# Optimization experiments

Hardware: AMD Instinct MI355X
Metric: run time of the kernel (lower is better)

Reference implementation:

```python
import jax, jax.numpy as jnp
import numpy as np
import math

D_MODEL = 768
N_HEADS = 12
D_HEAD = D_MODEL // N_HEADS


def setup_inputs() -> dict:
    key = jax.random.key(0)
    ks = jax.random.split(key, 5)
    x = jax.random.normal(ks[0], (2, 4096, D_MODEL), dtype=jnp.float32)
    s = 1.0 / math.sqrt(D_MODEL)
    W_qkv = jax.random.normal(ks[1], (D_MODEL, 3 * D_MODEL), dtype=jnp.float32) * s
    b_qkv = jnp.zeros((3 * D_MODEL,), dtype=jnp.float32)
    W_out = jax.random.normal(ks[2], (D_MODEL, D_MODEL), dtype=jnp.float32) * s
    b_out = jnp.zeros((D_MODEL,), dtype=jnp.float32)
    return {"x": x, "W_qkv": W_qkv, "b_qkv": b_qkv, "W_out": W_out, "b_out": b_out}


def reference(x, W_qkv, b_qkv, W_out, b_out):
    B, T, C = x.shape
    H, Dh = N_HEADS, D_HEAD
    qkv = x @ W_qkv + b_qkv                      # [B,T,3C]
    q, k, v = jnp.split(qkv, 3, axis=-1)
    q = q.reshape(B, T, H, Dh).transpose(0, 2, 1, 3)  # [B,H,T,Dh]
    k = k.reshape(B, T, H, Dh).transpose(0, 2, 1, 3)
    v = v.reshape(B, T, H, Dh).transpose(0, 2, 1, 3)
    att = jnp.einsum('bhqd,bhkd->bhqk', q, k) * (1.0 / math.sqrt(Dh))
    causal = jnp.tril(jnp.ones((T, T), dtype=bool))
    att = jnp.where(causal, att, -jnp.inf)
    att = jax.nn.softmax(att, axis=-1)
    out = jnp.einsum('bhqk,bhkd->bhqd', att, v)  # [B,H,T,Dh]
    out = out.transpose(0, 2, 1, 3).reshape(B, T, C)
    return out @ W_out + b_out
```

## Files before the change

kernel.cpp:

```cpp
#include <hip/hip_runtime.h>
#include <hip/hip_bf16.h>
#include <cstdint>

#define NH 12
#define DH 64
#define TSEQ 4096
#define BATCH 2
#define CDIM 768
#define MROWS (BATCH*TSEQ)

typedef __bf16 bf16x8 __attribute__((ext_vector_type(8)));
typedef __bf16 bf16x4 __attribute__((ext_vector_type(4)));
typedef bf16x8 bf16x8_a __attribute__((may_alias));
typedef bf16x4 bf16x4_a __attribute__((may_alias));
typedef float f32x4 __attribute__((ext_vector_type(4)));

__device__ __forceinline__ uint16_t f2bu(float f) {
  uint32_t u = __float_as_uint(f);
  u += 0x7fffu + ((u >> 16) & 1u);
  return (uint16_t)(u >> 16);
}

__device__ __forceinline__ float bu2f(uint16_t x) {
  return __uint_as_float(((uint32_t)x) << 16);
}

__device__ __forceinline__ void gload_lds16(const void* g, void* l) {
  __builtin_amdgcn_global_load_lds(
      (const __attribute__((address_space(1))) void*)g,
      (__attribute__((address_space(3))) void*)l, 16, 0, 0);
}

__global__ void cast_f32_bf16(const float* __restrict__ in, uint16_t* __restrict__ out, int n4) {
  int i = blockIdx.x * blockDim.x + threadIdx.x;
  int stride = gridDim.x * blockDim.x;
  for (; i < n4; i += stride) {
    float4 v = ((const float4*)in)[i];
    ushort4 o;
    o.x = f2bu(v.x); o.y = f2bu(v.y); o.z = f2bu(v.z); o.w = f2bu(v.w);
    ((ushort4*)out)[i] = o;
  }
}

__global__ void transpose_cast(const float* __restrict__ w, uint16_t* __restrict__ wt, int K, int N) {
  __shared__ float tile[32][33];
  int kb = blockIdx.x * 32, nb = blockIdx.y * 32;
  int tx = threadIdx.x & 31, ty = threadIdx.x >> 5;
  #pragma unroll
  for (int r = ty; r < 32; r += 8) tile[r][tx] = w[(size_t)(kb + r) * N + nb + tx];
  __syncthreads();
  #pragma unroll
  for (int r = ty; r < 32; r += 8) wt[(size_t)(nb + r) * K + kb + tx] = f2bu(tile[tx][r]);
}

__global__ __launch_bounds__(256) void gemm_qkv(
    const uint16_t* __restrict__ A, const uint16_t* __restrict__ Bt,
    const float* __restrict__ bias,
    uint16_t* __restrict__ q, uint16_t* __restrict__ k, uint16_t* __restrict__ v,
    int N, int K) {
  __shared__ uint16_t As[128 * 32];
  __shared__ uint16_t Bs[128 * 32];
  int tid = threadIdx.x;
  int w = tid >> 6, l = tid & 63;
  int lg = l >> 4, lr = l & 15;
  int mb = blockIdx.x * 128, nb = blockIdx.y * 128;
  int wr = (w >> 1) * 64, wc = (w & 1) * 64;
  f32x4 acc[4][4] = {};
  int srow = tid >> 2, scol = (tid & 3) * 8;
  const uint16_t* Ag = A + (size_t)(mb + srow) * K + scol;
  const uint16_t* Bg = Bt + (size_t)(nb + srow) * K + scol;
  char* AsB = (char*)As + (size_t)w * 1024;
  char* BsB = (char*)Bs + (size_t)w * 1024;
  size_t rowskip = (size_t)64 * K;
  for (int kb = 0; kb < K; kb += 32) {
    __syncthreads();
    gload_lds16(Ag + kb, AsB);
    gload_lds16(Ag + kb + rowskip, AsB + 4096);
    gload_lds16(Bg + kb, BsB);
    gload_lds16(Bg + kb + rowskip, BsB + 4096);
    __syncthreads();
    bf16x8 af[4], bfr[4];
    #pragma unroll
    for (int i = 0; i < 4; ++i)
      af[i] = *(const bf16x8_a*)(const void*)(As + (wr + i * 16 + lr) * 32 + lg * 8);
    #pragma unroll
    for (int i = 0; i < 4; ++i)
      bfr[i] = *(const bf16x8_a*)(const void*)(Bs + (wc + i * 16 + lr) * 32 + lg * 8);
    #pragma unroll
    for (int mi = 0; mi < 4; ++mi)
      #pragma unroll
      for (int ni = 0; ni < 4; ++ni)
        acc[mi][ni] = __builtin_amdgcn_mfma_f32_16x16x32_bf16(af[mi], bfr[ni], acc[mi][ni], 0, 0, 0);
  }
  #pragma unroll
  for (int mi = 0; mi < 4; ++mi) {
    #pragma unroll
    for (int ni = 0; ni < 4; ++ni) {
      int gm0 = mb + wr + mi * 16 + lg * 4;
      int gn = nb + wc + ni * 16 + lr;
      int which = gn / CDIM;
      int cc = gn - which * CDIM;
      int hh = cc >> 6, d = cc & 63;
      float bs = bias[gn];
      if (which == 2) {
        int b0 = gm0 >> 12, t0 = gm0 & 4095;
        ushort4 pk;
        pk.x = f2bu(acc[mi][ni][0] + bs);
        pk.y = f2bu(acc[mi][ni][1] + bs);
        pk.z = f2bu(acc[mi][ni][2] + bs);
        pk.w = f2bu(acc[mi][ni][3] + bs);
        *(ushort4*)&v[(((size_t)(b0 * NH + hh)) * DH + d) * TSEQ + t0] = pk;
      } else {
        uint16_t* dst = which ? k : q;
        float sc = which ? 1.0f : 0.1803368801111204f;
        #pragma unroll
        for (int j = 0; j < 4; ++j) {
          int gm = gm0 + j;
          int bb = gm >> 12, t = gm & 4095;
          float val = (acc[mi][ni][j] + bs) * sc;
          dst[(((size_t)(bb * NH + hh)) * TSEQ + t) * DH + d] = f2bu(val);
        }
      }
    }
  }
}

__global__ __launch_bounds__(256) void gemm_out(
    const uint16_t* __restrict__ A, const uint16_t* __restrict__ Bt,
    const float* __restrict__ bias, float* __restrict__ outf, int N, int K) {
  __shared__ uint16_t As[128 * 32];
  __shared__ uint16_t Bs[64 * 32];
  int tid = threadIdx.x;
  int w = tid >> 6, l = tid & 63;
  int lg = l >> 4, lr = l & 15;
  int mb = blockIdx.x * 128, nb = blockIdx.y * 64;
  int wr = w * 32;
  f32x4 acc[2][4] = {};
  int srow = tid >> 2, scol = (tid & 3) * 8;
  const uint16_t* Ag = A + (size_t)(mb + srow) * K + scol;
  const uint16_t* Bg = Bt + (size_t)(nb + srow) * K + scol;
  char* AsB = (char*)As + (size_t)w * 1024;
  char* BsB = (char*)Bs + (size_t)w * 1024;
  size_t rowskip = (size_t)64 * K;
  for (int kb = 0; kb < K; kb += 32) {
    __syncthreads();
    gload_lds16(Ag + kb, AsB);
    gload_lds16(Ag + kb + rowskip, AsB + 4096);
    gload_lds16(Bg + kb, BsB);
    __syncthreads();
    bf16x8 af[2], bfr[4];
    #pragma unroll
    for (int i = 0; i < 2; ++i)
      af[i] = *(const bf16x8_a*)(const void*)(As + (wr + i * 16 + lr) * 32 + lg * 8);
    #pragma unroll
    for (int i = 0; i < 4; ++i)
      bfr[i] = *(const bf16x8_a*)(const void*)(Bs + (i * 16 + lr) * 32 + lg * 8);
    #pragma unroll
    for (int mi = 0; mi < 2; ++mi)
      #pragma unroll
      for (int ni = 0; ni < 4; ++ni)
        acc[mi][ni] = __builtin_amdgcn_mfma_f32_16x16x32_bf16(af[mi], bfr[ni], acc[mi][ni], 0, 0, 0);
  }
  #pragma unroll
  for (int mi = 0; mi < 2; ++mi) {
    #pragma unroll
    for (int ni = 0; ni < 4; ++ni) {
      #pragma unroll
      for (int j = 0; j < 4; ++j) {
        int gm = mb + wr + mi * 16 + lg * 4 + j;
        int gn = nb + ni * 16 + lr;
        outf[(size_t)gm * N + gn] = acc[mi][ni][j] + bias[gn];
      }
    }
  }
}

__global__ __launch_bounds__(256) void attn_part(
    const uint16_t* __restrict__ Q, const uint16_t* __restrict__ K,
    const uint16_t* __restrict__ Vt, uint16_t* __restrict__ O,
    uint16_t* __restrict__ Pbuf, float* __restrict__ Plsum) {
  int gid = blockIdx.x;
  int widx = gid / 24, bh = gid - widx * 24;
  int qt, t0, t1, chunk;
  bool direct;
  if (widx < 32) {
    qt = 31 - (widx >> 1); chunk = widx & 1; direct = false;
    t0 = chunk ? (qt + 1) : 0;
    t1 = chunk ? (2 * qt + 1) : qt;
  } else {
    qt = 47 - widx; chunk = 0; direct = true;
    t0 = 0; t1 = 2 * qt + 1;
  }
  int b = bh / NH, hd = bh - b * NH;
  size_t base = (size_t)bh * TSEQ * DH;
  int tid = threadIdx.x, w = tid >> 6, lane = tid & 63;
  int lg = lane >> 4, lr = lane & 15;
  __shared__ __align__(16) uint16_t Ks[64 * 64];
  __shared__ __align__(16) uint16_t Vs[64 * 64];
  __shared__ uint16_t Ps[4][16 * 64];
  char* pw = (char*)Ps[w];
  int srow = tid >> 3;
  int schunk = (tid & 7) ^ (srow & 7);
  const uint16_t* Kg0 = K + base + (size_t)srow * DH + schunk * 8;
  const uint16_t* Vg0 = Vt + base + (size_t)srow * TSEQ + schunk * 8;
  char* KsB = (char*)Ks + w * 1024;
  char* VsB = (char*)Vs + w * 1024;
  int swzA = (lg ^ (lr & 7)) << 4;
  int swzB = swzA ^ 64;

  int qb = qt * 128;
  int qgA = qb + w * 16 + lr;
  int qgB = qgA + 64;
  bf16x8 qA0 = *(const bf16x8_a*)(const void*)(Q + base + (size_t)qgA * DH + lg * 8);
  bf16x8 qA1 = *(const bf16x8_a*)(const void*)(Q + base + (size_t)qgA * DH + 32 + lg * 8);
  bf16x8 qB0 = *(const bf16x8_a*)(const void*)(Q + base + (size_t)qgB * DH + lg * 8);
  bf16x8 qB1 = *(const bf16x8_a*)(const void*)(Q + base + (size_t)qgB * DH + 32 + lg * 8);
  f32x4 oA[4] = {}, oB[4] = {};
  float lA = 0.f, lB = 0.f;
  int lg4 = lg * 4;
  int pofs = (lg & 1) * 8;

  for (int t = t0; t <= t1; ++t) {
    __syncthreads();
    {
      const uint16_t* kg_ = Kg0 + (size_t)t * (64 * DH);
      const uint16_t* vg_ = Vg0 + (size_t)t * 64;
      gload_lds16(kg_,           KsB);
      gload_lds16(kg_ + 32 * DH, KsB + 4096);
      gload_lds16(vg_,                     VsB);
      gload_lds16(vg_ + (size_t)32 * TSEQ, VsB + 4096);
    }
    __syncthreads();
    bool doA = (t <= 2 * qt);
    int kb0 = t * 64;
    f32x4 sA[4], sB[4];
    __builtin_amdgcn_s_setprio(1);
    #pragma unroll
    for (int ni = 0; ni < 4; ++ni) {
      const char* kbp = (const char*)Ks + (ni * 16 + lr) * 128;
      bf16x8 kf0 = *(const bf16x8_a*)(kbp + swzA);
      bf16x8 kf1 = *(const bf16x8_a*)(kbp + swzB);
      f32x4 s = {};
      s = __builtin_amdgcn_mfma_f32_16x16x32_bf16(kf0, qB0, s, 0, 0, 0);
      s = __builtin_amdgcn_mfma_f32_16x16x32_bf16(kf1, qB1, s, 0, 0, 0);
      sB[ni] = s;
      if (doA) {
        f32x4 sa = {};
        sa = __builtin_amdgcn_mfma_f32_16x16x32_bf16(kf0, qA0, sa, 0, 0, 0);
        sa = __builtin_amdgcn_mfma_f32_16x16x32_bf16(kf1, qA1, sa, 0, 0, 0);
        sA[ni] = sa;
      }
    }
    __builtin_amdgcn_s_setprio(0);
    bf16x8 pfA0, pfA1;
    if (doA) {
      if (t == 2 * qt) {
        int thr = qgA - kb0 - lg4;
        #pragma unroll
        for (int ni = 0; ni < 4; ++ni)
          #pragma unroll
          for (int j = 0; j < 4; ++j)
            sA[ni][j] = (16 * ni + j <= thr) ? sA[ni][j] : -1e30f;
      }
      #pragma unroll
      for (int ni = 0; ni < 4; ++ni) {
        float p0 = __builtin_amdgcn_exp2f(sA[ni][0]);
        float p1 = __builtin_amdgcn_exp2f(sA[ni][1]);
        float p2 = __builtin_amdgcn_exp2f(sA[ni][2]);
        float p3 = __builtin_amdgcn_exp2f(sA[ni][3]);
        lA += (p0 + p1) + (p2 + p3);
        bf16x4 pk;
        pk[0] = (__bf16)p0; pk[1] = (__bf16)p1; pk[2] = (__bf16)p2; pk[3] = (__bf16)p3;
        int chunkc = (2 * ni + (lg >> 1)) ^ (lr & 7);
        *(bf16x4_a*)(pw + lr * 128 + chunkc * 16 + pofs) = pk;
      }
      pfA0 = *(const bf16x8_a*)(pw + lr * 128 + swzA);
      pfA1 = *(const bf16x8_a*)(pw + lr * 128 + swzB);
    }
    {
      if (t == 2 * qt + 1) {
        int thr = qgB - kb0 - lg4;
        #pragma unroll
        for (int ni = 0; ni < 4; ++ni)
          #pragma unroll
          for (int j = 0; j < 4; ++j)
            sB[ni][j] = (16 * ni + j <= thr) ? sB[ni][j] : -1e30f;
      }
      #pragma unroll
      for (int ni = 0; ni < 4; ++ni) {
        float p0 = __builtin_amdgcn_exp2f(sB[ni][0]);
        float p1 = __builtin_amdgcn_exp2f(sB[ni][1]);
        float p2 = __builtin_amdgcn_exp2f(sB[ni][2]);
        float p3 = __builtin_amdgcn_exp2f(sB[ni][3]);
        lB += (p0 + p1) + (p2 + p3);
        bf16x4 pk;
        pk[0] = (__bf16)p0; pk[1] = (__bf16)p1; pk[2] = (__bf16)p2; pk[3] = (__bf16)p3;
        int chunkc = (2 * ni + (lg >> 1)) ^ (lr & 7);
        *(bf16x4_a*)(pw + lr * 128 + chunkc * 16 + pofs) = pk;
      }
    }
    bf16x8 pfB0 = *(const bf16x8_a*)(pw + lr * 128 + swzA);
    bf16x8 pfB1 = *(const bf16x8_a*)(pw + lr * 128 + swzB);
    __builtin_amdgcn_s_setprio(1);
    #pragma unroll
    for (int nd = 0; nd < 4; ++nd) {
      const char* vb = (const char*)Vs + (nd * 16 + lr) * 128;
      bf16x8 vf0 = *(const bf16x8_a*)(vb + swzA);
      bf16x8 vf1 = *(const bf16x8_a*)(vb + swzB);
      oB[nd] = __builtin_amdgcn_mfma_f32_16x16x32_bf16(pfB0, vf0, oB[nd], 0, 0, 0);
      oB[nd] = __builtin_amdgcn_mfma_f32_16x16x32_bf16(pfB1, vf1, oB[nd], 0, 0, 0);
      if (doA) {
        oA[nd] = __builtin_amdgcn_mfma_f32_16x16x32_bf16(pfA0, vf0, oA[nd], 0, 0, 0);
        oA[nd] = __builtin_amdgcn_mfma_f32_16x16x32_bf16(pfA1, vf1, oA[nd], 0, 0, 0);
      }
    }
    __builtin_amdgcn_s_setprio(0);
  }

  lA += __shfl_xor(lA, 16, 64); lA += __shfl_xor(lA, 32, 64);
  lB += __shfl_xor(lB, 16, 64); lB += __shfl_xor(lB, 32, 64);
  if (direct) {
    float riA = 1.0f / lA, riB = 1.0f / lB;
    #pragma unroll
    for (int j = 0; j < 4; ++j) {
      float rvA = __shfl(riA, (lane & 48) | (lg4 + j), 64);
      float rvB = __shfl(riB, (lane & 48) | (lg4 + j), 64);
      int tA = qb + w * 16 + lg4 + j;
      size_t pA = (size_t)(b * TSEQ + tA) * CDIM + hd * DH + lr;
      size_t pB = pA + (size_t)64 * CDIM;
      #pragma unroll
      for (int nd = 0; nd < 4; ++nd) {
        O[pA + nd * 16] = f2bu(oA[nd][j] * rvA);
        O[pB + nd * 16] = f2bu(oB[nd][j] * rvB);
      }
    }
  } else {
    int pidx = (bh << 4) + (qt - 16);
    uint16_t* Pb = Pbuf + ((size_t)pidx * 2 + chunk) * 8192;
    float* Pl = Plsum + ((size_t)pidx * 2 + chunk) * 128;
    #pragma unroll
    for (int j = 0; j < 4; ++j) {
      int qlA = w * 16 + lg4 + j;
      #pragma unroll
      for (int nd = 0; nd < 4; ++nd) {
        Pb[qlA * 64 + nd * 16 + lr] = f2bu(oA[nd][j]);
        Pb[(64 + qlA) * 64 + nd * 16 + lr] = f2bu(oB[nd][j]);
      }
    }
    if (lane < 16) {
      Pl[w * 16 + lane] = lA;
      Pl[64 + w * 16 + lane] = lB;
    }
  }
}

__global__ __launch_bounds__(256) void attn_reduce(
    const uint16_t* __restrict__ Pbuf, const float* __restrict__ Plsum,
    uint16_t* __restrict__ O) {
  int pidx = blockIdx.x;
  int bh = pidx >> 4, qrel = pidx & 15;
  int qt = 16 + qrel;
  int b = bh / NH, hd = bh - b * NH;
  int d = threadIdx.x & 63, qo = threadIdx.x >> 6;
  const uint16_t* p0 = Pbuf + (size_t)pidx * 2 * 8192;
  const uint16_t* p1 = p0 + 8192;
  const float* l0 = Plsum + (size_t)pidx * 2 * 128;
  const float* l1 = l0 + 128;
  #pragma unroll 4
  for (int q = qo; q < 128; q += 4) {
    float li = 1.0f / (l0[q] + l1[q]);
    float s = bu2f(p0[q * 64 + d]) + bu2f(p1[q * 64 + d]);
    int t = qt * 128 + q;
    O[(size_t)(b * TSEQ + t) * CDIM + hd * DH + d] = f2bu(s * li);
  }
}

extern "C" void kernel_launch(void* const* d_in, const int* in_sizes, int n_in,
                              void* d_out, int out_size, void* d_ws, size_t ws_size,
                              hipStream_t stream) {
  const float* x    = (const float*)d_in[0];
  const float* Wqkv = (const float*)d_in[1];
  const float* bqkv = (const float*)d_in[2];
  const float* Wout = (const float*)d_in[3];
  const float* bout = (const float*)d_in[4];
  float* out = (float*)d_out;
  char* ws = (char*)d_ws;

  uint16_t* Xb    = (uint16_t*)(ws + 0);
  uint16_t* Wqkvt = (uint16_t*)(ws + 12582912);
  uint16_t* Woutt = (uint16_t*)(ws + 16121856);
  uint16_t* Qb    = (uint16_t*)(ws + 17301504);
  uint16_t* Kb    = (uint16_t*)(ws + 29884416);
  uint16_t* Vtb   = (uint16_t*)(ws + 42467328);
  uint16_t* Ob    = (uint16_t*)(ws + 55050240);
  uint16_t* Pbuf  = Xb;
  float*    Plsum = (float*)Wqkvt;

  cast_f32_bf16<<<2048, 256, 0, stream>>>(x, Xb, (MROWS * CDIM) / 4);
  transpose_cast<<<dim3(24, 72), 256, 0, stream>>>(Wqkv, Wqkvt, 768, 2304);
  transpose_cast<<<dim3(24, 24), 256, 0, stream>>>(Wout, Woutt, 768, 768);
  gemm_qkv<<<dim3(64, 18), 256, 0, stream>>>(Xb, Wqkvt, bqkv, Qb, Kb, Vtb, 2304, 768);
  attn_part<<<1152, 256, 0, stream>>>(Qb, Kb, Vtb, Ob, Pbuf, Plsum);
  attn_reduce<<<384, 256, 0, stream>>>(Pbuf, Plsum, Ob);
  gemm_out<<<dim3(64, 12), 256, 0, stream>>>(Ob, Woutt, bout, out, 768, 768);
}
```

Baseline: 191.5 us.

## Split causal attention KV range into up to three chunks for load balance

Replaces the fixed two-way KV split for the upper half of query tiles with a graded scheme. The largest query tiles are split three ways, the middle ones two ways, and the smallest run unsplit, raising the block count from 1152 to 1512 so per-block work is more even. Chunk 0 now writes its unnormalized partial straight into the output buffer, and the reduce kernel reads it back and adds the remaining chunks, which avoids one partial-buffer round trip. The cost is more partial writes and reads and a bf16 round-trip of the unnormalized partial, which may lose some accuracy.

```diff
diff --git a/kernel.cpp b/kernel.cpp
--- a/kernel.cpp
+++ b/kernel.cpp
@@ -175,22 +175,28 @@
   }
 }
 
+__device__ __forceinline__ int lbase_qt(int qt) {
+  return (qt < 22) ? (qt - 11) * 2 : 22 + (qt - 22) * 3;
+}
+__device__ __forceinline__ int ebase_qt(int qt) {
+  return (qt < 22) ? (qt - 11) : 11 + (qt - 22) * 2;
+}
+
 __global__ __launch_bounds__(256) void attn_part(
     const uint16_t* __restrict__ Q, const uint16_t* __restrict__ K,
     const uint16_t* __restrict__ Vt, uint16_t* __restrict__ O,
-    uint16_t* __restrict__ Pbuf, float* __restrict__ Plsum) {
+    uint16_t* __restrict__ Pbuf, float* __restrict__ Pl) {
   int gid = blockIdx.x;
   int widx = gid / 24, bh = gid - widx * 24;
-  int qt, t0, t1, chunk;
-  bool direct;
-  if (widx < 32) {
-    qt = 31 - (widx >> 1); chunk = widx & 1; direct = false;
-    t0 = chunk ? (qt + 1) : 0;
-    t1 = chunk ? (2 * qt + 1) : qt;
-  } else {
-    qt = 47 - widx; chunk = 0; direct = true;
-    t0 = 0; t1 = 2 * qt + 1;
-  }
+  int qt, c, nch;
+  if (widx < 30) { qt = 31 - widx / 3; c = widx % 3; nch = 3; }
+  else if (widx < 52) { int u = widx - 30; qt = 21 - (u >> 1); c = u & 1; nch = 2; }
+  else { qt = 62 - widx; c = 0; nch = 1; }
+  int ntile = 2 * qt + 2;
+  int L = (ntile + nch - 1) / nch;
+  int t0 = c * L;
+  int t1 = min(ntile - 1, t0 + L - 1);
+
   int b = bh / NH, hd = bh - b * NH;
   size_t base = (size_t)bh * TSEQ * DH;
   int tid = threadIdx.x, w = tid >> 6, lane = tid & 63;
@@ -319,7 +325,7 @@
 
   lA += __shfl_xor(lA, 16, 64); lA += __shfl_xor(lA, 32, 64);
   lB += __shfl_xor(lB, 16, 64); lB += __shfl_xor(lB, 32, 64);
-  if (direct) {
+  if (nch == 1) {
     float riA = 1.0f / lA, riB = 1.0f / lB;
     #pragma unroll
     for (int j = 0; j < 4; ++j) {
@@ -335,43 +341,57 @@
       }
     }
   } else {
-    int pidx = (bh << 4) + (qt - 16);
-    uint16_t* Pb = Pbuf + ((size_t)pidx * 2 + chunk) * 8192;
-    float* Pl = Plsum + ((size_t)pidx * 2 + chunk) * 128;
-    #pragma unroll
-    for (int j = 0; j < 4; ++j) {
-      int qlA = w * 16 + lg4 + j;
-      #pragma unroll
-      for (int nd = 0; nd < 4; ++nd) {
-        Pb[qlA * 64 + nd * 16 + lr] = f2bu(oA[nd][j]);
-        Pb[(64 + qlA) * 64 + nd * 16 + lr] = f2bu(oB[nd][j]);
-      }
-    }
+    float* pl = Pl + (size_t)(bh * 64 + lbase_qt(qt) + c) * 128;
     if (lane < 16) {
-      Pl[w * 16 + lane] = lA;
-      Pl[64 + w * 16 + lane] = lB;
+      pl[w * 16 + lane] = lA;
+      pl[64 + w * 16 + lane] = lB;
+    }
+    if (c == 0) {
+      #pragma unroll
+      for (int j = 0; j < 4; ++j) {
+        int tA = qb + w * 16 + lg4 + j;
+        size_t pA = (size_t)(b * TSEQ + tA) * CDIM + hd * DH + lr;
+        size_t pB = pA + (size_t)64 * CDIM;
+        #pragma unroll
+        for (int nd = 0; nd < 4; ++nd) {
+          O[pA + nd * 16] = f2bu(oA[nd][j]);
+          O[pB + nd * 16] = f2bu(oB[nd][j]);
+        }
+      }
+    } else {
+      uint16_t* Pb = Pbuf + (size_t)(bh * 31 + ebase_qt(qt) + (c - 1)) * 8192;
+      #pragma unroll
+      for (int j = 0; j < 4; ++j) {
+        int qlA = w * 16 + lg4 + j;
+        #pragma unroll
+        for (int nd = 0; nd < 4; ++nd) {
+          Pb[qlA * 64 + nd * 16 + lr] = f2bu(oA[nd][j]);
+          Pb[(64 + qlA) * 64 + nd * 16 + lr] = f2bu(oB[nd][j]);
+        }
+      }
     }
   }
 }
 
 __global__ __launch_bounds__(256) void attn_reduce(
-    const uint16_t* __restrict__ Pbuf, const float* __restrict__ Plsum,
+    const uint16_t* __restrict__ Pbuf, const float* __restrict__ Pl,
     uint16_t* __restrict__ O) {
-  int pidx = blockIdx.x;
-  int bh = pidx >> 4, qrel = pidx & 15;
-  int qt = 16 + qrel;
+  int rid = blockIdx.x;
+  int bh = rid / 21, qt = 11 + (rid - bh * 21);
+  int nch = (qt >= 22) ? 3 : 2;
   int b = bh / NH, hd = bh - b * NH;
   int d = threadIdx.x & 63, qo = threadIdx.x >> 6;
-  const uint16_t* p0 = Pbuf + (size_t)pidx * 2 * 8192;
-  const uint16_t* p1 = p0 + 8192;
-  const float* l0 = Plsum + (size_t)pidx * 2 * 128;
-  const float* l1 = l0 + 128;
+  const float* pl = Pl + (size_t)(bh * 64 + lbase_qt(qt)) * 128;
+  const uint16_t* pb = Pbuf + (size_t)(bh * 31 + ebase_qt(qt)) * 8192;
   #pragma unroll 4
   for (int q = qo; q < 128; q += 4) {
-    float li = 1.0f / (l0[q] + l1[q]);
-    float s = bu2f(p0[q * 64 + d]) + bu2f(p1[q * 64 + d]);
+    float lsum = pl[q] + pl[128 + q];
+    if (nch == 3) lsum += pl[256 + q];
     int t = qt * 128 + q;
-    O[(size_t)(b * TSEQ + t) * CDIM + hd * DH + d] = f2bu(s * li);
+    size_t po = (size_t)(b * TSEQ + t) * CDIM + hd * DH + d;
+    float s = bu2f(O[po]) + bu2f(pb[q * 64 + d]);
+    if (nch == 3) s += bu2f(pb[8192 + q * 64 + d]);
+    O[po] = f2bu(s / lsum);
   }
 }
 
@@ -394,13 +414,13 @@
   uint16_t* Vtb   = (uint16_t*)(ws + 42467328);
   uint16_t* Ob    = (uint16_t*)(ws + 55050240);
   uint16_t* Pbuf  = Xb;
-  float*    Plsum = (float*)Wqkvt;
+  float*    Pl    = (float*)Wqkvt;
 
   cast_f32_bf16<<<2048, 256, 0, stream>>>(x, Xb, (MROWS * CDIM) / 4);
   transpose_cast<<<dim3(24, 72), 256, 0, stream>>>(Wqkv, Wqkvt, 768, 2304);
   transpose_cast<<<dim3(24, 24), 256, 0, stream>>>(Wout, Woutt, 768, 768);
   gemm_qkv<<<dim3(64, 18), 256, 0, stream>>>(Xb, Wqkvt, bqkv, Qb, Kb, Vtb, 2304, 768);
-  attn_part<<<1152, 256, 0, stream>>>(Qb, Kb, Vtb, Ob, Pbuf, Plsum);
-  attn_reduce<<<384, 256, 0, stream>>>(Pbuf, Plsum, Ob);
+  attn_part<<<1512, 256, 0, stream>>>(Qb, Kb, Vtb, Ob, Pbuf, Pl);
+  attn_reduce<<<504, 256, 0, stream>>>(Pbuf, Pl, Ob);
   gemm_out<<<dim3(64, 12), 256, 0, stream>>>(Ob, Woutt, bout, out, 768, 768);
 }
```

Result: slower. 197.7 us (+3.3%).
